# Performance work log

Hardware: AMD Instinct MI355X
Metric: run time of the kernel (lower is better)

## Reference

```python
import jax, jax.numpy as jnp
import numpy as np

B, T, IN = 256, 60, 520
GATE_IN = 8                      # 5 + 3, hard-coded in module
MOE_RAW = IN - GATE_IN           # 512
MOE_IN = MOE_RAW + GATE_IN * T   # 992
HID = MOE_RAW + (GATE_IN * T) // 2  # 752 (Python precedence: a + b*c//2)
OUT = 512
E = 8


def _uniform(key, shape, bound):
    return jax.random.uniform(key, shape, jnp.float32, -bound, bound)


def setup_inputs() -> dict:
    key = jax.random.key(0)
    ks = jax.random.split(key, 16)
    X = jax.random.normal(ks[0], (B, T, IN), jnp.float32)
    # GRU: 2 layers, hidden = E, gate order r,z,n (torch convention)
    gb = 1.0 / np.sqrt(E)
    Wih0 = _uniform(ks[1], (3 * E, GATE_IN), gb)
    Whh0 = _uniform(ks[2], (3 * E, E), gb)
    bih0 = _uniform(ks[3], (3 * E,), gb)
    bhh0 = _uniform(ks[4], (3 * E,), gb)
    Wih1 = _uniform(ks[5], (3 * E, E), gb)
    Whh1 = _uniform(ks[6], (3 * E, E), gb)
    bih1 = _uniform(ks[7], (3 * E,), gb)
    bhh1 = _uniform(ks[8], (3 * E,), gb)
    # Expert banks: glorot-style uniform as in init_params, zero biases
    def bank(k, i, o):
        wb = np.sqrt(6.0 / (i * o))
        return _uniform(k, (E, i, o), wb)
    w1 = bank(ks[9], MOE_IN, HID); b1 = jnp.zeros((E, HID), jnp.float32)
    w2 = bank(ks[10], HID, HID);   b2 = jnp.zeros((E, HID), jnp.float32)
    w3 = bank(ks[11], HID, OUT);   b3 = jnp.zeros((E, OUT), jnp.float32)
    return dict(X=X, Wih0=Wih0, Whh0=Whh0, bih0=bih0, bhh0=bhh0,
                Wih1=Wih1, Whh1=Whh1, bih1=bih1, bhh1=bhh1,
                w1=w1, b1=b1, w2=w2, b2=b2, w3=w3, b3=b3)


def _gru_layer(x, Wih, Whh, bih, bhh):
    # x: [B, T, in] -> outputs [B, T, H]
    H = Whh.shape[1]
    h0 = jnp.zeros((x.shape[0], H), x.dtype)

    def step(h, xt):
        gi = xt @ Wih.T + bih
        gh = h @ Whh.T + bhh
        ir, iz, i_n = jnp.split(gi, 3, axis=-1)
        hr, hz, h_n = jnp.split(gh, 3, axis=-1)
        r = jax.nn.sigmoid(ir + hr)
        z = jax.nn.sigmoid(iz + hz)
        n = jnp.tanh(i_n + r * h_n)
        h_new = (1.0 - z) * n + z * h
        return h_new, h_new

    _, ys = jax.lax.scan(step, h0, jnp.swapaxes(x, 0, 1))
    return jnp.swapaxes(ys, 0, 1)


def _blend_layer(x, coef, w, b):
    # per-sample weight synthesis + apply: same math as
    # sum(coef[...,None,None]*w[None],dim=1) then sum(x[...,None]*W,dim=1)+b
    Wb = jnp.einsum('be,eih->bih', coef, w)   # [B, in, out]
    bb = coef @ b                              # [B, out]
    return jnp.einsum('bi,bih->bh', x, Wb) + bb


def reference(X, Wih0, Whh0, bih0, bhh0, Wih1, Whh1, bih1, bhh1,
              w1, b1, w2, b2, w3, b3):
    Xg = X[:, :, MOE_RAW:]                                   # [B, T, 8]
    Xm = jnp.concatenate(
        [X[:, -1, :MOE_RAW], X[:, :, -GATE_IN:].reshape(X.shape[0], -1)], -1)
    # gating: 2-layer GRU, softmax on last step of layer 2
    h1 = _gru_layer(Xg, Wih0, Whh0, bih0, bhh0)
    h2 = _gru_layer(h1, Wih1, Whh1, bih1, bhh1)
    Omega = jax.nn.softmax(h2[:, -1, :], axis=-1)            # [B, E]
    # expert MLP with blended per-sample weights
    a = jax.nn.elu(_blend_layer(Xm, Omega, w1, b1))
    a = jax.nn.elu(_blend_layer(a, Omega, w2, b2))
    Y = _blend_layer(a, Omega, w3, b3)
    return Y
```

## Files before the change

### kernel.cpp

```cpp
#include <hip/hip_runtime.h>
#include <cstdint>
#include <cstddef>

typedef __attribute__((ext_vector_type(8))) short short8;
typedef __attribute__((ext_vector_type(8))) unsigned short ushort8;
typedef __attribute__((ext_vector_type(4))) float f32x4;

#define AS1Q const __attribute__((address_space(1)))
#define AS3Q __attribute__((address_space(3)))

constexpr int T_N = 60, IN_N = 520, MOE_RAW_N = 512, MOE_IN_N = 992;
constexpr int HID_N = 752, E_N = 8;
constexpr int K2_N = 6016;
constexpr int KA_N = 1024;
constexpr int SPLITK = 20;
constexpr int PN = 768;

static __device__ __forceinline__ unsigned short f2bf(float f) {
  unsigned int u = __float_as_uint(f);
  return (unsigned short)((u + 0x7fffu + ((u >> 16) & 1u)) >> 16);
}
static __device__ __forceinline__ float sigf(float x) {
  return __fdividef(1.f, 1.f + __expf(-x));
}
static __device__ __forceinline__ float tanh_fast(float x) {
  return 2.f * __fdividef(1.f, 1.f + __expf(-2.f * x)) - 1.f;
}

template<int R>
static __device__ __forceinline__ float rotf(float v) {
  return __int_as_float(__builtin_amdgcn_update_dpp(
      0, __float_as_int(v), 0x120 | R, 0xF, 0xF, true));
}
static __device__ __forceinline__ void rot8(float (&d)[8], float v) {
  d[0] = v;
  d[1] = rotf<1>(v); d[2] = rotf<2>(v); d[3] = rotf<3>(v);
  d[4] = rotf<4>(v); d[5] = rotf<5>(v); d[6] = rotf<6>(v); d[7] = rotf<7>(v);
}

__global__ __launch_bounds__(256)
void xm_prep(const float* __restrict__ X, unsigned short* __restrict__ XmBf)
{
  const int i = blockIdx.x * 256 + threadIdx.x;
  const int b = blockIdx.y;
  const float* Xb = X + (size_t)b * (T_N * IN_N);
  float v = 0.f;
  if (i < MOE_RAW_N) {
    v = Xb[(T_N - 1) * IN_N + i];
  } else if (i < MOE_IN_N) {
    const int q = i - MOE_RAW_N;
    v = Xb[(q >> 3) * IN_N + MOE_RAW_N + (q & 7)];
  }
  XmBf[(size_t)b * KA_N + (i ^ ((b & 7) << 3))] = f2bf(v);
}

__global__ __launch_bounds__(256, 1)
void fused_gru_gemm1(const float* __restrict__ X,
                     const float* __restrict__ Wih0, const float* __restrict__ Whh0,
                     const float* __restrict__ bih0, const float* __restrict__ bhh0,
                     const float* __restrict__ Wih1, const float* __restrict__ Whh1,
                     const float* __restrict__ bih1, const float* __restrict__ bhh1,
                     const unsigned short* __restrict__ XmBf,
                     const float* __restrict__ w1,
                     float* __restrict__ Y1, float* __restrict__ Omega)
{
  __shared__ union SM {
    struct { unsigned short Al[2][256][64]; unsigned short Bl[2][64][64]; } g;
    struct { float xl[T_N][256]; float wl[12][8][8]; } r;
  } sm;

  const int tid  = threadIdx.x;
  const int lane = tid & 63;
  const int wave = tid >> 6;

  if (blockIdx.x < 16) {
    const int j = tid & 7;
    const int b = blockIdx.x * 16 + (tid >> 4);

    const float* xsrc = X + (size_t)b * (T_N * IN_N) + MOE_RAW_N + j;
#pragma unroll
    for (int t = 0; t < T_N; ++t) {
      __builtin_amdgcn_global_load_lds((AS1Q unsigned int*)(xsrc + t * IN_N),
                                       (AS3Q unsigned int*)&sm.r.xl[t][wave * 64], 4, 0, 0);
    }

    const int got = __builtin_amdgcn_update_dpp(0, j, 0x121, 0xF, 0xF, true);
    const bool plus = (got == ((j + 1) & 7));

    if (tid < 64) {
      const int fj = tid >> 3, fr = tid & 7;
      const int fi = plus ? ((fj + fr) & 7) : ((fj - fr) & 7);
      const int idx = plus ? ((fj + fr) & 7) : ((fj - fr) & 7);
      (void)fi;
      const float* Wm[4] = {Wih0, Whh0, Wih1, Whh1};
#pragma unroll
      for (int mat = 0; mat < 4; ++mat)
#pragma unroll
        for (int gg = 0; gg < 3; ++gg)
          sm.r.wl[mat * 3 + gg][fj][fr] = Wm[mat][(gg * 8 + fj) * 8 + idx];
    }

    const float br0 = bih0[j] + bhh0[j], bz0 = bih0[8 + j] + bhh0[8 + j];
    const float bin0 = bih0[16 + j],     bhn0 = bhh0[16 + j];
    const float br1 = bih1[j] + bhh1[j], bz1 = bih1[8 + j] + bhh1[8 + j];
    const float bin1 = bih1[16 + j],     bhn1 = bhh1[16 + j];

    __syncthreads();

    float h1 = 0.f, h2 = 0.f;
    float xcur = sm.r.xl[0][tid];

    auto dot8 = [&](int m, const float (&rv)[8], float& accA, float& accB) {
      const f32x4 w0 = *(const f32x4*)&sm.r.wl[m][j][0];
      const f32x4 w1v = *(const f32x4*)&sm.r.wl[m][j][4];
#pragma unroll
      for (int q = 0; q < 4; ++q) { accA += w0[q] * rv[q]; accB += w1v[q] * rv[4 + q]; }
    };

#pragma unroll 1
    for (int t = 0; t <= T_N; ++t) {
      const float xnext = sm.r.xl[(t + 1 < T_N) ? t + 1 : T_N - 1][tid];

      float rx[8];  rot8(rx, xcur);
      float rh1[8]; rot8(rh1, h1);
      float rh2[8]; rot8(rh2, h2);

      float grA = br0, gzA = bz0, gnA = bin0, hnA = bhn0;
      float grB = 0.f, gzB = 0.f, gnB = 0.f, hnB = 0.f;
      dot8(0, rx, grA, grB); dot8(1, rx, gzA, gzB); dot8(2, rx, gnA, gnB);
      dot8(3, rh1, grA, grB); dot8(4, rh1, gzA, gzB); dot8(5, rh1, hnA, hnB);
      float h1n;
      {
        const float r0 = sigf(grA + grB), z0 = sigf(gzA + gzB);
        const float n0 = tanh_fast((gnA + gnB) + r0 * (hnA + hnB));
        h1n = (1.f - z0) * n0 + z0 * h1;
      }

      float grA1 = br1, gzA1 = bz1, gnA1 = bin1, hnA1 = bhn1;
      float grB1 = 0.f, gzB1 = 0.f, gnB1 = 0.f, hnB1 = 0.f;
      dot8(6, rh1, grA1, grB1); dot8(7, rh1, gzA1, gzB1); dot8(8, rh1, gnA1, gnB1);
      dot8(9, rh2, grA1, grB1); dot8(10, rh2, gzA1, gzB1); dot8(11, rh2, hnA1, hnB1);
      float h2n;
      {
        const float r1 = sigf(grA1 + grB1), z1 = sigf(gzA1 + gzB1);
        const float n1 = tanh_fast((gnA1 + gnB1) + r1 * (hnA1 + hnB1));
        h2n = (1.f - z1) * n1 + z1 * h2;
      }

      h1 = h1n;
      h2 = (t == 0) ? 0.f : h2n;
      xcur = xnext;
    }

    float rv[8]; rot8(rv, h2);
    float m = rv[0];
#pragma unroll
    for (int r = 1; r < 8; ++r) m = fmaxf(m, rv[r]);
    const float ej = __expf(h2 - m);
    float re[8]; rot8(re, ej);
    float sden = 0.f;
#pragma unroll
    for (int r = 0; r < 8; ++r) sden += re[r];
    if (!(tid & 8)) Omega[b * 8 + j] = __fdividef(ej, sden);
    return;
  }

  const int bid = blockIdx.x - 16;
  const int sp  = bid / 96;
  const int rr0 = bid - sp * 96;
  const int e   = rr0 & 7;
  const int nt  = rr0 >> 3;
  const int n0  = nt * 64;
  const int kt0 = sp * 8, kt1 = kt0 + 8;

  const int r15 = lane & 15, hi4 = lane >> 4, r7 = lane & 7;

  const unsigned short* Abase = XmBf + (size_t)(wave * 64 + (lane >> 3)) * KA_N + (lane & 7) * 8;
  const int bn = lane;
  const int kq = wave;
  const bool nvalid = (n0 + bn) < HID_N;
  const float* Bbase = w1 + ((size_t)e * MOE_IN_N + kq * 16) * HID_N + (n0 + bn);

  f32x4 acc[4][4];
  const f32x4 zero4 = {0.f, 0.f, 0.f, 0.f};
#pragma unroll
  for (int mi = 0; mi < 4; ++mi)
#pragma unroll
    for (int ni = 0; ni < 4; ++ni) acc[mi][ni] = zero4;

  auto stage = [&](int bufi, int kt) {
    const unsigned short* ga = Abase + kt * 64;
#pragma unroll
    for (int it = 0; it < 8; ++it) {
      __builtin_amdgcn_global_load_lds(
          (AS1Q unsigned int*)(ga + (size_t)it * 8 * KA_N),
          (AS3Q unsigned int*)&sm.g.Al[bufi][wave * 64 + it * 8][0],
          16, 0, 0);
    }
    const int kbase = kt * 64 + kq * 16;
    const float* gb = Bbase + (size_t)kt * 64 * HID_N;
    float v[16];
#pragma unroll
    for (int jj = 0; jj < 16; ++jj)
      v[jj] = (nvalid && (kbase + jj) < MOE_IN_N) ? gb[(size_t)jj * HID_N] : 0.f;
    ushort8 p0, p1;
#pragma unroll
    for (int jj = 0; jj < 8; ++jj) { p0[jj] = f2bf(v[jj]); p1[jj] = f2bf(v[jj + 8]); }
    const int sl0 = ((kq * 2) ^ (bn & 7)) * 8;
    const int sl1 = ((kq * 2 + 1) ^ (bn & 7)) * 8;
    *(ushort8*)&sm.g.Bl[bufi][bn][sl0] = p0;
    *(ushort8*)&sm.g.Bl[bufi][bn][sl1] = p1;
  };

  auto compute = [&](int bufi) {
#pragma unroll
    for (int ki = 0; ki < 2; ++ki) {
      const int ch = ((ki * 4 + hi4) ^ r7) * 8;
      short8 af[4], bfv[4];
#pragma unroll
      for (int mi = 0; mi < 4; ++mi)
        af[mi] = *(const short8*)&sm.g.Al[bufi][wave * 64 + mi * 16 + r15][ch];
#pragma unroll
      for (int ni = 0; ni < 4; ++ni)
        bfv[ni] = *(const short8*)&sm.g.Bl[bufi][ni * 16 + r15][ch];
#pragma unroll
      for (int mi = 0; mi < 4; ++mi)
#pragma unroll
        for (int ni = 0; ni < 4; ++ni)
          acc[mi][ni] = __builtin_amdgcn_mfma_f32_16x16x32_bf16(af[mi], bfv[ni], acc[mi][ni], 0, 0, 0);
    }
  };

  stage(0, kt0);
  __syncthreads();
  int buf = 0;
  for (int kt = kt0; kt < kt1; ++kt) {
    if (kt + 1 < kt1) stage(buf ^ 1, kt + 1);
    compute(buf);
    __syncthreads();
    buf ^= 1;
  }

  float* Pp = Y1 + ((size_t)(sp * 8 + e) * 256) * PN + n0;
#pragma unroll
  for (int mi = 0; mi < 4; ++mi) {
    const int row = wave * 64 + mi * 16 + hi4 * 4;
#pragma unroll
    for (int ni = 0; ni < 4; ++ni) {
#pragma unroll
      for (int rq = 0; rq < 4; ++rq)
        Pp[(size_t)(row + rq) * PN + ni * 16 + r15] = acc[mi][ni][rq];
    }
  }
}

__global__ __launch_bounds__(256)
void reduce1_mix(const float* __restrict__ Y1, const float* __restrict__ Omega,
                 const float* __restrict__ bias, unsigned short* __restrict__ xnext)
{
  const int n = blockIdx.x * 256 + threadIdx.x;
  const int b = blockIdx.y;
  if (n >= HID_N) return;
  float om[8];
#pragma unroll
  for (int e = 0; e < 8; ++e) om[e] = Omega[b * 8 + e];
  float acc = 0.f, bs = 0.f;
#pragma unroll
  for (int e = 0; e < 8; ++e) {
    const float ye = Y1[((size_t)e * 256 + b) * PN + n]
                   + Y1[((size_t)(8 + e) * 256 + b) * PN + n];
    acc += om[e] * ye;
    bs  += om[e] * bias[(size_t)e * HID_N + n];
  }
  const float y = acc + bs;
  const float a = (y > 0.f) ? y : expm1f(y);
  const int swz = (b & 7) << 3;
  unsigned short* row = xnext + (size_t)b * K2_N;
#pragma unroll
  for (int e = 0; e < 8; ++e)
    row[(e * HID_N + n) ^ swz] = f2bf(om[e] * a);
}

__global__ __launch_bounds__(256)
void gemm_splitk(const unsigned short* __restrict__ A,
                 const float* __restrict__ Bw,
                 float* __restrict__ P,
                 int K, int N, int NPAD)
{
  __shared__ unsigned short Al[2][256][64];
  __shared__ unsigned short Bl[2][64][64];

  const int tid = threadIdx.x;
  const int lane = tid & 63;
  const int wave = tid >> 6;
  const int nt = blockIdx.x, sp = blockIdx.y;
  const int n0 = nt * 64;
  const int KT = K >> 6;
  const int kt0 = (KT * sp) / SPLITK;
  const int kt1 = (KT * (sp + 1)) / SPLITK;

  const int r15 = lane & 15, hi4 = lane >> 4, r7 = lane & 7;

  const unsigned short* Abase = A + (size_t)(wave * 64 + (lane >> 3)) * K + (lane & 7) * 8;
  const int bn = lane;
  const int kq = wave;
  const bool nvalid = (n0 + bn) < N;
  const float* Bbase = Bw + (size_t)(kq * 16) * N + (n0 + bn);

  f32x4 acc[4][4];
  const f32x4 zero4 = {0.f, 0.f, 0.f, 0.f};
#pragma unroll
  for (int mi = 0; mi < 4; ++mi)
#pragma unroll
    for (int ni = 0; ni < 4; ++ni) acc[mi][ni] = zero4;

  auto stage = [&](int bufi, int kt) {
    const unsigned short* ga = Abase + kt * 64;
#pragma unroll
    for (int it = 0; it < 8; ++it) {
      __builtin_amdgcn_global_load_lds(
          (AS1Q unsigned int*)(ga + (size_t)it * 8 * K),
          (AS3Q unsigned int*)&Al[bufi][wave * 64 + it * 8][0],
          16, 0, 0);
    }
    const float* gb = Bbase + (size_t)kt * 64 * N;
    float v[16];
#pragma unroll
    for (int jj = 0; jj < 16; ++jj) v[jj] = nvalid ? gb[(size_t)jj * N] : 0.f;
    ushort8 p0, p1;
#pragma unroll
    for (int jj = 0; jj < 8; ++jj) { p0[jj] = f2bf(v[jj]); p1[jj] = f2bf(v[jj + 8]); }
    const int sl0 = ((kq * 2) ^ (bn & 7)) * 8;
    const int sl1 = ((kq * 2 + 1) ^ (bn & 7)) * 8;
    *(ushort8*)&Bl[bufi][bn][sl0] = p0;
    *(ushort8*)&Bl[bufi][bn][sl1] = p1;
  };

  auto compute = [&](int bufi) {
#pragma unroll
    for (int ki = 0; ki < 2; ++ki) {
      const int ch = ((ki * 4 + hi4) ^ r7) * 8;
      short8 af[4], bfv[4];
#pragma unroll
      for (int mi = 0; mi < 4; ++mi)
        af[mi] = *(const short8*)&Al[bufi][wave * 64 + mi * 16 + r15][ch];
#pragma unroll
      for (int ni = 0; ni < 4; ++ni)
        bfv[ni] = *(const short8*)&Bl[bufi][ni * 16 + r15][ch];
#pragma unroll
      for (int mi = 0; mi < 4; ++mi)
#pragma unroll
        for (int ni = 0; ni < 4; ++ni)
          acc[mi][ni] = __builtin_amdgcn_mfma_f32_16x16x32_bf16(af[mi], bfv[ni], acc[mi][ni], 0, 0, 0);
    }
  };

  stage(0, kt0);
  __syncthreads();
  int buf = 0;
  for (int kt = kt0; kt < kt1; ++kt) {
    if (kt + 1 < kt1) stage(buf ^ 1, kt + 1);
    compute(buf);
    __syncthreads();
    buf ^= 1;
  }

  float* Pp = P + (size_t)sp * 256 * NPAD + n0;
#pragma unroll
  for (int mi = 0; mi < 4; ++mi) {
    const int row = wave * 64 + mi * 16 + hi4 * 4;
#pragma unroll
    for (int ni = 0; ni < 4; ++ni) {
#pragma unroll
      for (int rq = 0; rq < 4; ++rq)
        Pp[(size_t)(row + rq) * NPAD + ni * 16 + r15] = acc[mi][ni][rq];
    }
  }
}

__global__ __launch_bounds__(256)
void reduce_mix_kernel(const float* __restrict__ P, const float* __restrict__ Omega,
                       const float* __restrict__ bias, unsigned short* __restrict__ xnext,
                       float* __restrict__ Yout, int N, int NPAD)
{
  const int n = blockIdx.x * 256 + threadIdx.x;
  const int b = blockIdx.y;
  if (n >= N) return;
  float acc = 0.f;
#pragma unroll 4
  for (int s = 0; s < SPLITK; ++s) acc += P[((size_t)s * 256 + b) * NPAD + n];
  float om[8];
#pragma unroll
  for (int e = 0; e < 8; ++e) om[e] = Omega[b * 8 + e];
  float bs = 0.f;
#pragma unroll
  for (int e = 0; e < 8; ++e) bs += om[e] * bias[(size_t)e * N + n];
  float y = acc + bs;
  if (Yout) { Yout[(size_t)b * N + n] = y; return; }
  float a = (y > 0.f) ? y : expm1f(y);
  const int swz = (b & 7) << 3;
  unsigned short* row = xnext + (size_t)b * K2_N;
#pragma unroll
  for (int e = 0; e < 8; ++e)
    row[(e * HID_N + n) ^ swz] = f2bf(om[e] * a);
}

extern "C" void kernel_launch(void* const* d_in, const int* in_sizes, int n_in,
                              void* d_out, int out_size, void* d_ws, size_t ws_size,
                              hipStream_t stream) {
  const float* X    = (const float*)d_in[0];
  const float* Wih0 = (const float*)d_in[1];
  const float* Whh0 = (const float*)d_in[2];
  const float* bih0 = (const float*)d_in[3];
  const float* bhh0 = (const float*)d_in[4];
  const float* Wih1 = (const float*)d_in[5];
  const float* Whh1 = (const float*)d_in[6];
  const float* bih1 = (const float*)d_in[7];
  const float* bhh1 = (const float*)d_in[8];
  const float* w1   = (const float*)d_in[9];
  const float* b1   = (const float*)d_in[10];
  const float* w2   = (const float*)d_in[11];
  const float* b2   = (const float*)d_in[12];
  const float* w3   = (const float*)d_in[13];
  const float* b3   = (const float*)d_in[14];

  char* ws = (char*)d_ws;
  float* Omega         = (float*)ws;
  unsigned short* XmBf = (unsigned short*)(ws + 8192);
  unsigned short* xt2  = (unsigned short*)(ws + 532480);
  unsigned short* xt3  = (unsigned short*)(ws + 3612672);
  float* Y1            = (float*)(ws + 6692864);
  float* P             = (float*)(ws + 19275776);

  xm_prep<<<dim3(4, 256), 256, 0, stream>>>(X, XmBf);

  fused_gru_gemm1<<<208, 256, 0, stream>>>(X, Wih0, Whh0, bih0, bhh0,
                                           Wih1, Whh1, bih1, bhh1,
                                           XmBf, w1, Y1, Omega);

  reduce1_mix<<<dim3(3, 256), 256, 0, stream>>>(Y1, Omega, b1, xt2);

  gemm_splitk<<<dim3(12, SPLITK), 256, 0, stream>>>(xt2, w2, P, K2_N, HID_N, 768);
  reduce_mix_kernel<<<dim3(3, 256), 256, 0, stream>>>(P, Omega, b2, xt3, nullptr, HID_N, 768);

  gemm_splitk<<<dim3(8, SPLITK), 256, 0, stream>>>(xt3, w3, P, K2_N, 512, 512);
  reduce_mix_kernel<<<dim3(2, 256), 256, 0, stream>>>(P, Omega, b3, nullptr, (float*)d_out, 512, 512);
}
```

Before: 80.87 us.

## Pre-convert w2/w3 to swizzled bf16 in spare blocks of GRU kernel

Adds 48 extra blocks to the fused GRU/GEMM1 kernel. They convert the w2 and w3 expert banks into transposed, swizzled bf16 tiles in workspace, running alongside the latency-bound GRU. The split-K GEMMs then load B tiles straight into LDS with global_load_lds instead of doing strided fp32 loads and converting in-kernel. This removes redundant conversion and uncoalesced B loads. In exchange it spends extra memory traffic on the conversion every call, and the extra blocks compete with the GEMM1 blocks for CUs.

```diff
diff --git a/kernel.cpp b/kernel.cpp
--- a/kernel.cpp
+++ b/kernel.cpp
@@ -15,6 +15,8 @@
 constexpr int KA_N = 1024;
 constexpr int SPLITK = 20;
 constexpr int PN = 768;
+constexpr int NT_W2 = 94 * 12;
+constexpr int NT_W3 = 94 * 8;
 
 static __device__ __forceinline__ unsigned short f2bf(float f) {
   unsigned int u = __float_as_uint(f);
@@ -62,17 +64,52 @@
                      const float* __restrict__ bih1, const float* __restrict__ bhh1,
                      const unsigned short* __restrict__ XmBf,
                      const float* __restrict__ w1,
+                     const float* __restrict__ w2, const float* __restrict__ w3,
+                     unsigned short* __restrict__ B2sw2,
+                     unsigned short* __restrict__ B2sw3,
                      float* __restrict__ Y1, float* __restrict__ Omega)
 {
   __shared__ union SM {
     struct { unsigned short Al[2][256][64]; unsigned short Bl[2][64][64]; } g;
     struct { float xl[T_N][256]; float wl[12][8][8]; } r;
+    struct { unsigned short tl[64][66]; } c;
   } sm;
 
   const int tid  = threadIdx.x;
   const int lane = tid & 63;
   const int wave = tid >> 6;
 
+  if (blockIdx.x >= 208) {
+    const int cid = blockIdx.x - 208;
+    for (int tile = cid; tile < NT_W2 + NT_W3; tile += 48) {
+      const float* W; unsigned short* Dst; int N, kt, ntile;
+      if (tile < NT_W2) { W = w2; Dst = B2sw2; N = HID_N; kt = tile / 12; ntile = tile % 12; }
+      else { const int t2 = tile - NT_W2; W = w3; Dst = B2sw3; N = 512; kt = t2 / 8; ntile = t2 % 8; }
+      const int n0 = ntile * 64, k0 = kt * 64;
+      const int nl = tid & 63;
+#pragma unroll
+      for (int p = 0; p < 16; ++p) {
+        const int kl = (tid >> 6) + p * 4;
+        const float v = (n0 + nl < N) ? W[(size_t)(k0 + kl) * N + n0 + nl] : 0.f;
+        sm.c.tl[kl][nl] = f2bf(v);
+      }
+      __syncthreads();
+      const int nl2 = tid >> 2, q = tid & 3;
+      ushort8 o0, o1;
+#pragma unroll
+      for (int m = 0; m < 16; ++m) {
+        const int cc = (q * 16 + m) >> 3, j = m & 7;
+        const unsigned short val = sm.c.tl[((cc ^ (nl2 & 7)) << 3) + j][nl2];
+        if (m < 8) o0[m] = val; else o1[m - 8] = val;
+      }
+      unsigned short* drow = Dst + (size_t)(n0 + nl2) * K2_N + k0 + q * 16;
+      *(ushort8*)drow = o0;
+      *(ushort8*)(drow + 8) = o1;
+      __syncthreads();
+    }
+    return;
+  }
+
   if (blockIdx.x < 16) {
     const int j = tid & 7;
     const int b = blockIdx.x * 16 + (tid >> 4);
@@ -89,9 +126,7 @@
 
     if (tid < 64) {
       const int fj = tid >> 3, fr = tid & 7;
-      const int fi = plus ? ((fj + fr) & 7) : ((fj - fr) & 7);
       const int idx = plus ? ((fj + fr) & 7) : ((fj - fr) & 7);
-      (void)fi;
       const float* Wm[4] = {Wih0, Whh0, Wih1, Whh1};
 #pragma unroll
       for (int mat = 0; mat < 4; ++mat)
@@ -283,7 +318,7 @@
 
 __global__ __launch_bounds__(256)
 void gemm_splitk(const unsigned short* __restrict__ A,
-                 const float* __restrict__ Bw,
+                 const unsigned short* __restrict__ Bsw,
                  float* __restrict__ P,
                  int K, int N, int NPAD)
 {
@@ -302,10 +337,7 @@
   const int r15 = lane & 15, hi4 = lane >> 4, r7 = lane & 7;
 
   const unsigned short* Abase = A + (size_t)(wave * 64 + (lane >> 3)) * K + (lane & 7) * 8;
-  const int bn = lane;
-  const int kq = wave;
-  const bool nvalid = (n0 + bn) < N;
-  const float* Bbase = Bw + (size_t)(kq * 16) * N + (n0 + bn);
+  const unsigned short* Bbase = Bsw + (size_t)(n0 + (wave * 2) * 8 + (lane >> 3)) * K2_N + (lane & 7) * 8;
 
   f32x4 acc[4][4];
   const f32x4 zero4 = {0.f, 0.f, 0.f, 0.f};
@@ -323,17 +355,14 @@
           (AS3Q unsigned int*)&Al[bufi][wave * 64 + it * 8][0],
           16, 0, 0);
     }
-    const float* gb = Bbase + (size_t)kt * 64 * N;
-    float v[16];
-#pragma unroll
-    for (int jj = 0; jj < 16; ++jj) v[jj] = nvalid ? gb[(size_t)jj * N] : 0.f;
-    ushort8 p0, p1;
-#pragma unroll
-    for (int jj = 0; jj < 8; ++jj) { p0[jj] = f2bf(v[jj]); p1[jj] = f2bf(v[jj + 8]); }
-    const int sl0 = ((kq * 2) ^ (bn & 7)) * 8;
-    const int sl1 = ((kq * 2 + 1) ^ (bn & 7)) * 8;
-    *(ushort8*)&Bl[bufi][bn][sl0] = p0;
-    *(ushort8*)&Bl[bufi][bn][sl1] = p1;
+    const unsigned short* gbB = Bbase + kt * 64;
+#pragma unroll
+    for (int it = 0; it < 2; ++it) {
+      __builtin_amdgcn_global_load_lds(
+          (AS1Q unsigned int*)(gbB + (size_t)it * 8 * K2_N),
+          (AS3Q unsigned int*)&Bl[bufi][(wave * 2 + it) * 8][0],
+          16, 0, 0);
+    }
   };
 
   auto compute = [&](int bufi) {
@@ -425,24 +454,27 @@
   const float* b3   = (const float*)d_in[14];
 
   char* ws = (char*)d_ws;
-  float* Omega         = (float*)ws;
-  unsigned short* XmBf = (unsigned short*)(ws + 8192);
-  unsigned short* xt2  = (unsigned short*)(ws + 532480);
-  unsigned short* xt3  = (unsigned short*)(ws + 3612672);
-  float* Y1            = (float*)(ws + 6692864);
-  float* P             = (float*)(ws + 19275776);
+  float* Omega          = (float*)ws;
+  unsigned short* XmBf  = (unsigned short*)(ws + 8192);
+  unsigned short* xt2   = (unsigned short*)(ws + 532480);
+  unsigned short* xt3   = (unsigned short*)(ws + 3612672);
+  float* Y1             = (float*)(ws + 6692864);
+  float* P              = (float*)(ws + 19275776);
+  unsigned short* B2sw2 = (unsigned short*)(ws + 35004416);
+  unsigned short* B2sw3 = (unsigned short*)(ws + 44244992);
 
   xm_prep<<<dim3(4, 256), 256, 0, stream>>>(X, XmBf);
 
-  fused_gru_gemm1<<<208, 256, 0, stream>>>(X, Wih0, Whh0, bih0, bhh0,
+  fused_gru_gemm1<<<256, 256, 0, stream>>>(X, Wih0, Whh0, bih0, bhh0,
                                            Wih1, Whh1, bih1, bhh1,
-                                           XmBf, w1, Y1, Omega);
+                                           XmBf, w1, w2, w3, B2sw2, B2sw3,
+                                           Y1, Omega);
 
   reduce1_mix<<<dim3(3, 256), 256, 0, stream>>>(Y1, Omega, b1, xt2);
 
-  gemm_splitk<<<dim3(12, SPLITK), 256, 0, stream>>>(xt2, w2, P, K2_N, HID_N, 768);
+  gemm_splitk<<<dim3(12, SPLITK), 256, 0, stream>>>(xt2, B2sw2, P, K2_N, HID_N, 768);
   reduce_mix_kernel<<<dim3(3, 256), 256, 0, stream>>>(P, Omega, b2, xt3, nullptr, HID_N, 768);
 
-  gemm_splitk<<<dim3(8, SPLITK), 256, 0, stream>>>(xt3, w3, P, K2_N, 512, 512);
+  gemm_splitk<<<dim3(8, SPLITK), 256, 0, stream>>>(xt3, B2sw3, P, K2_N, 512, 512);
   reduce_mix_kernel<<<dim3(2, 256), 256, 0, stream>>>(P, Omega, b3, nullptr, (float*)d_out, 512, 512);
 }
```

After: 167.9 us. 2.08x slower.
